# Kernel tuning notes

Measured on AMD Instinct MI355X. Metric: run time of the kernel, lower is better.

## Reference

```python
import jax, jax.numpy as jnp
import numpy as np

B, TE, TD, D, U = 8, 256, 256, 256, 256


def setup_inputs() -> dict:
    key = jax.random.key(0)
    k1, k2, k3, k4, k5 = jax.random.split(key, 5)
    glorot = lambda k, shape: jax.random.uniform(
        k, shape, jnp.float32,
        -np.sqrt(6.0 / (shape[0] + shape[1])), np.sqrt(6.0 / (shape[0] + shape[1])))
    return {
        "en_seq": jax.random.normal(k1, (B, TE, D), jnp.float32),
        "de_seq": jax.random.normal(k2, (B, TD, D), jnp.float32),
        "w_en": glorot(k3, (D, U)),
        "w_de": glorot(k4, (D, U)),
        "nu": glorot(k5, (U, 1)),
    }


def reference(en_seq, de_seq, w_en, w_de, nu):
    # Additive co-attention scores.
    ae = jnp.einsum('bte,eu->btu', en_seq, w_en)          # (B, Te, U)
    ad = jnp.einsum('bsd,du->bsu', de_seq, w_de)          # (B, Td, U)
    # co_m[b, td, te, u] = ae[b, te, u] + ad[b, td, u]  (matches K.repeat / repeat_elements layout)
    co = jnp.tanh(ad[:, :, None, :] + ae[:, None, :, :])  # (B, Td, Te, U)
    mu = jnp.einsum('bstu,ul->bst', co, nu)               # (B, Td, Te)
    alphas = jax.nn.softmax(mu, axis=-1)                  # softmax over en time
    max_mu = jnp.max(mu, axis=-1)                         # (B, Td)
    max_alphas = jax.nn.softmax(max_mu, axis=-1)          # softmax over de time
    h_hat = jnp.sum(de_seq * max_alphas[..., None], axis=1)  # (B, Dd)
    sum_en = jnp.einsum('bst,bte->bse', alphas, en_seq)      # (B, Td, De)
    output = jnp.concatenate(
        [de_seq, sum_en, de_seq * sum_en, de_seq * h_hat[:, None, :]], axis=-1)
    return output  # (B, Td, 4*D)
```

## Files before the change

### kernel.cpp

```cpp
#include <hip/hip_runtime.h>

#define B_   8
#define TE_  256
#define TD_  256
#define D_   256
#define U_   256

#define EET_OFF   0
#define ED_OFF    524288
#define ALPHA_OFF 1048576
#define MAXMU_OFF 1572864
#define HH_OFF    1574912

__device__ __forceinline__ float fexp2(float x) {
#if __has_builtin(__builtin_amdgcn_exp2f)
  return __builtin_amdgcn_exp2f(x);
#else
  return exp2f(x);
#endif
}
__device__ __forceinline__ float frcp(float x) {
#if __has_builtin(__builtin_amdgcn_rcpf)
  return __builtin_amdgcn_rcpf(x);
#else
  return 1.0f / x;
#endif
}
__device__ __forceinline__ float rdlane(float v, int l) {
  return __int_as_float(__builtin_amdgcn_readlane(__float_as_int(v), l));
}

#define LOG2E_F 1.4426950408889634f
#define TWO_LOG2E_F 2.8853900817779268f

__global__ __launch_bounds__(256) void coatt_k1_proj(
    const float* __restrict__ en, const float* __restrict__ de,
    const float* __restrict__ w_en, const float* __restrict__ w_de,
    float* __restrict__ ws) {
  const int bi = blockIdx.x;
  const int which = bi >> 8;
  const float* __restrict__ A = which ? de : en;
  const float* __restrict__ W = which ? w_de : w_en;
  const int r0 = (bi & 255) * 8;
  const int tid = threadIdx.x;
  const int w = tid >> 6, lane = tid & 63;
  const int rowW = r0 + w * 2;
  const int u4 = lane * 4;

  const float* __restrict__ Arow = A + (size_t)(rowW + (lane >> 5)) * D_ + (lane & 31);

  float4 acc0 = {0, 0, 0, 0}, acc1 = {0, 0, 0, 0};
  for (int k0 = 0; k0 < D_; k0 += 32) {
    const float areg = Arow[k0];
#pragma unroll
    for (int h = 0; h < 2; ++h) {
      float4 wv[16];
#pragma unroll
      for (int k = 0; k < 16; ++k)
        wv[k] = *(const float4*)&W[(k0 + h * 16 + k) * U_ + u4];
#pragma unroll
      for (int k = 0; k < 16; ++k) {
        const float a0 = rdlane(areg, h * 16 + k);
        const float a1 = rdlane(areg, 32 + h * 16 + k);
        acc0.x = fmaf(a0, wv[k].x, acc0.x);
        acc0.y = fmaf(a0, wv[k].y, acc0.y);
        acc0.z = fmaf(a0, wv[k].z, acc0.z);
        acc0.w = fmaf(a0, wv[k].w, acc0.w);
        acc1.x = fmaf(a1, wv[k].x, acc1.x);
        acc1.y = fmaf(a1, wv[k].y, acc1.y);
        acc1.z = fmaf(a1, wv[k].z, acc1.z);
        acc1.w = fmaf(a1, wv[k].w, acc1.w);
      }
    }
  }

  __shared__ float TT[8][257];
  if (which) {
    float* __restrict__ out = ws + ED_OFF;
    float4 o0, o1;
    o0.x = fexp2(acc0.x * TWO_LOG2E_F); o0.y = fexp2(acc0.y * TWO_LOG2E_F);
    o0.z = fexp2(acc0.z * TWO_LOG2E_F); o0.w = fexp2(acc0.w * TWO_LOG2E_F);
    o1.x = fexp2(acc1.x * TWO_LOG2E_F); o1.y = fexp2(acc1.y * TWO_LOG2E_F);
    o1.z = fexp2(acc1.z * TWO_LOG2E_F); o1.w = fexp2(acc1.w * TWO_LOG2E_F);
    *(float4*)&out[(rowW + 0) * U_ + u4] = o0;
    *(float4*)&out[(rowW + 1) * U_ + u4] = o1;
  } else {
    const float* a0p = (const float*)&acc0;
    const float* a1p = (const float*)&acc1;
#pragma unroll
    for (int j = 0; j < 4; ++j) {
      TT[w * 2 + 0][u4 + j] = fexp2(a0p[j] * TWO_LOG2E_F);
      TT[w * 2 + 1][u4 + j] = fexp2(a1p[j] * TWO_LOG2E_F);
    }
    __syncthreads();
    const int b = r0 >> 8, t0 = r0 & 255;
    float v[8];
#pragma unroll
    for (int k = 0; k < 8; ++k) v[k] = TT[k][tid];
    float* __restrict__ p = ws + EET_OFF + (size_t)(b * U_ + tid) * TE_ + t0;
    float4 q0, q1;
    q0.x = v[0]; q0.y = v[1]; q0.z = v[2]; q0.w = v[3];
    q1.x = v[4]; q1.y = v[5]; q1.z = v[6]; q1.w = v[7];
    *(float4*)&p[0] = q0;
    *(float4*)&p[4] = q1;
  }
}

__global__ __launch_bounds__(256) void coatt_k2_mu(
    const float* __restrict__ nu, float* __restrict__ ws) {
  float* __restrict__ alphas = ws + ALPHA_OFF;
  float* __restrict__ maxmu = ws + MAXMU_OFF;
  const int b = blockIdx.y;
  const int sBase = blockIdx.x * 4;
  const int tid = threadIdx.x;
  const int w = tid >> 6, lane = tid & 63;
  const float* __restrict__ Ee_b = ws + EET_OFF + (size_t)b * U_ * TE_ + tid;
  const float* __restrict__ EdCoop =
      ws + ED_OFF + (size_t)(b * TD_ + sBase + (lane >> 4)) * U_ + (lane & 15);

  float acc0 = 0.f, acc1 = 0.f, acc2 = 0.f, acc3 = 0.f;
  for (int c = 0; c < 4; ++c) {
    const float nureg = nu[c * 64 + lane];
#pragma unroll
    for (int q = 0; q < 4; ++q) {
      const int u0 = c * 64 + q * 16;
      const float edreg = EdCoop[u0];
      float ee[16];
#pragma unroll
      for (int j = 0; j < 16; ++j) ee[j] = Ee_b[(u0 + j) * TE_];
#pragma unroll
      for (int j = 0; j < 16; ++j) {
        const float nv = rdlane(nureg, q * 16 + j);
        const float e0 = rdlane(edreg, j);
        const float e1 = rdlane(edreg, 16 + j);
        const float e2 = rdlane(edreg, 32 + j);
        const float e3 = rdlane(edreg, 48 + j);
        acc0 = fmaf(nv, frcp(fmaf(e0, ee[j], 1.0f)), acc0);
        acc1 = fmaf(nv, frcp(fmaf(e1, ee[j], 1.0f)), acc1);
        acc2 = fmaf(nv, frcp(fmaf(e2, ee[j], 1.0f)), acc2);
        acc3 = fmaf(nv, frcp(fmaf(e3, ee[j], 1.0f)), acc3);
      }
    }
  }
  float v[4] = {-2.f * acc0, -2.f * acc1, -2.f * acc2, -2.f * acc3};
  __shared__ float part[4][4];
  float m[4];
#pragma unroll
  for (int s = 0; s < 4; ++s) {
    m[s] = v[s];
#pragma unroll
    for (int off = 32; off > 0; off >>= 1) m[s] = fmaxf(m[s], __shfl_xor(m[s], off));
    if (lane == 0) part[s][w] = m[s];
  }
  __syncthreads();
#pragma unroll
  for (int s = 0; s < 4; ++s)
    m[s] = fmaxf(fmaxf(part[s][0], part[s][1]), fmaxf(part[s][2], part[s][3]));
  __syncthreads();
  float e[4], sm[4];
#pragma unroll
  for (int s = 0; s < 4; ++s) {
    e[s] = fexp2((v[s] - m[s]) * LOG2E_F);
    sm[s] = e[s];
#pragma unroll
    for (int off = 32; off > 0; off >>= 1) sm[s] += __shfl_xor(sm[s], off);
    if (lane == 0) part[s][w] = sm[s];
  }
  __syncthreads();
  float* __restrict__ al = alphas + (size_t)(b * TD_ + sBase) * TE_;
#pragma unroll
  for (int s = 0; s < 4; ++s) {
    const float tot = (part[s][0] + part[s][1]) + (part[s][2] + part[s][3]);
    al[s * TE_ + tid] = e[s] * frcp(tot);
  }
  if (tid == 0) {
#pragma unroll
    for (int s = 0; s < 4; ++s) maxmu[b * TD_ + sBase + s] = m[s];
  }
}

__global__ __launch_bounds__(256) void coatt_k3_hhat(
    const float* __restrict__ de, float* __restrict__ ws) {
  const float* __restrict__ maxmu = ws + MAXMU_OFF;
  float* __restrict__ hhat = ws + HH_OFF;
  const int b = blockIdx.y;
  const int dBase = blockIdx.x * 32;
  const int tid = threadIdx.x;
  const int w = tid >> 6, lane = tid & 63;
  __shared__ float red[8];
  __shared__ float malpha[256];
  __shared__ float acc_red[256];
  const float v = maxmu[b * TD_ + tid];
  float m = v;
#pragma unroll
  for (int off = 32; off > 0; off >>= 1) m = fmaxf(m, __shfl_xor(m, off));
  if (lane == 0) red[w] = m;
  __syncthreads();
  m = fmaxf(fmaxf(red[0], red[1]), fmaxf(red[2], red[3]));
  const float e = fexp2((v - m) * LOG2E_F);
  float sm = e;
#pragma unroll
  for (int off = 32; off > 0; off >>= 1) sm += __shfl_xor(sm, off);
  if (lane == 0) red[4 + w] = sm;
  __syncthreads();
  sm = (red[4] + red[5]) + (red[6] + red[7]);
  malpha[tid] = e * frcp(sm);
  __syncthreads();
  const int dl = tid & 31, sg = tid >> 5;
  float acc = 0.f;
  for (int s = sg * 32; s < sg * 32 + 32; ++s)
    acc = fmaf(de[(b * TD_ + s) * D_ + dBase + dl], malpha[s], acc);
  acc_red[tid] = acc;
  __syncthreads();
  if (tid < 32) {
    float t = acc_red[tid];
#pragma unroll
    for (int g = 1; g < 8; ++g) t += acc_red[g * 32 + tid];
    hhat[b * D_ + dBase + tid] = t;
  }
}

__global__ __launch_bounds__(256) void coatt_k4_out(
    const float* __restrict__ en, const float* __restrict__ de,
    const float* __restrict__ ws, float* __restrict__ out) {
  const float* __restrict__ hhat = ws + HH_OFF;
  const int b = blockIdx.y;
  const int sBase = blockIdx.x * 4;
  const int tid = threadIdx.x;
  const int lane = tid & 63;
  const int d = tid;
  const float* __restrict__ alCoop =
      ws + ALPHA_OFF + (size_t)(b * TD_ + sBase + (lane >> 4)) * TE_ + (lane & 15);
  const float* __restrict__ en_b = en + (size_t)b * TE_ * D_ + d;

  float acc0 = 0.f, acc1 = 0.f, acc2 = 0.f, acc3 = 0.f;
  for (int t0 = 0; t0 < TE_; t0 += 16) {
    const float alreg = alCoop[t0];
    float env[16];
#pragma unroll
    for (int j = 0; j < 16; ++j) env[j] = en_b[(t0 + j) * D_];
#pragma unroll
    for (int j = 0; j < 16; ++j) {
      acc0 = fmaf(rdlane(alreg, j),      env[j], acc0);
      acc1 = fmaf(rdlane(alreg, 16 + j), env[j], acc1);
      acc2 = fmaf(rdlane(alreg, 32 + j), env[j], acc2);
      acc3 = fmaf(rdlane(alreg, 48 + j), env[j], acc3);
    }
  }
  const float hh = hhat[b * D_ + d];
  const float se[4] = {acc0, acc1, acc2, acc3};
#pragma unroll
  for (int s = 0; s < 4; ++s) {
    const float dd = de[(size_t)(b * TD_ + sBase + s) * D_ + d];
    float* o = out + (size_t)(b * TD_ + sBase + s) * (4 * D_);
    o[d] = dd;
    o[D_ + d] = se[s];
    o[2 * D_ + d] = dd * se[s];
    o[3 * D_ + d] = dd * hh;
  }
}

extern "C" void kernel_launch(void* const* d_in, const int* in_sizes, int n_in,
                              void* d_out, int out_size, void* d_ws, size_t ws_size,
                              hipStream_t stream) {
  (void)in_sizes; (void)n_in; (void)out_size; (void)ws_size;
  const float* en   = (const float*)d_in[0];
  const float* de   = (const float*)d_in[1];
  const float* w_en = (const float*)d_in[2];
  const float* w_de = (const float*)d_in[3];
  const float* nu   = (const float*)d_in[4];
  float* out = (float*)d_out;
  float* ws  = (float*)d_ws;

  coatt_k1_proj<<<dim3(512), 256, 0, stream>>>(en, de, w_en, w_de, ws);
  coatt_k2_mu<<<dim3(64, 8), 256, 0, stream>>>(nu, ws);
  coatt_k3_hhat<<<dim3(8, 8), 256, 0, stream>>>(de, ws);
  coatt_k4_out<<<dim3(64, 8), 256, 0, stream>>>(en, de, ws, out);
}
```

Before: 138.7 us.

## Fuse h_hat into output kernel and software-pipeline loads in all kernels

Removes the separate h_hat kernel. Each output block now recomputes the max-mu softmax and the weighted de-sum redundantly, which saves a launch and a dependency step but adds 256x256 extra reads per block. The projection, mu and output kernels gain register double-buffering so the next tile's loads are issued before the current tile's FMAs. Cross-lane readlane broadcasts are replaced with uniform float4 loads of Ed, nu and alpha, and launch bounds now ask for 2 blocks per SIMD.

```diff
diff --git a/kernel.cpp b/kernel.cpp
--- a/kernel.cpp
+++ b/kernel.cpp
@@ -10,7 +10,6 @@
 #define ED_OFF    524288
 #define ALPHA_OFF 1048576
 #define MAXMU_OFF 1572864
-#define HH_OFF    1574912
 
 __device__ __forceinline__ float fexp2(float x) {
 #if __has_builtin(__builtin_amdgcn_exp2f)
@@ -33,7 +32,7 @@
 #define LOG2E_F 1.4426950408889634f
 #define TWO_LOG2E_F 2.8853900817779268f
 
-__global__ __launch_bounds__(256) void coatt_k1_proj(
+__global__ __launch_bounds__(256, 2) void coatt_k1_proj(
     const float* __restrict__ en, const float* __restrict__ de,
     const float* __restrict__ w_en, const float* __restrict__ w_de,
     float* __restrict__ ws) {
@@ -50,28 +49,37 @@
   const float* __restrict__ Arow = A + (size_t)(rowW + (lane >> 5)) * D_ + (lane & 31);
 
   float4 acc0 = {0, 0, 0, 0}, acc1 = {0, 0, 0, 0};
-  for (int k0 = 0; k0 < D_; k0 += 32) {
-    const float areg = Arow[k0];
-#pragma unroll
-    for (int h = 0; h < 2; ++h) {
-      float4 wv[16];
-#pragma unroll
-      for (int k = 0; k < 16; ++k)
-        wv[k] = *(const float4*)&W[(k0 + h * 16 + k) * U_ + u4];
-#pragma unroll
-      for (int k = 0; k < 16; ++k) {
-        const float a0 = rdlane(areg, h * 16 + k);
-        const float a1 = rdlane(areg, 32 + h * 16 + k);
-        acc0.x = fmaf(a0, wv[k].x, acc0.x);
-        acc0.y = fmaf(a0, wv[k].y, acc0.y);
-        acc0.z = fmaf(a0, wv[k].z, acc0.z);
-        acc0.w = fmaf(a0, wv[k].w, acc0.w);
-        acc1.x = fmaf(a1, wv[k].x, acc1.x);
-        acc1.y = fmaf(a1, wv[k].y, acc1.y);
-        acc1.z = fmaf(a1, wv[k].z, acc1.z);
-        acc1.w = fmaf(a1, wv[k].w, acc1.w);
+  float areg = Arow[0];
+  float4 wbuf[8], wnxt[8];
+#pragma unroll
+  for (int j = 0; j < 8; ++j) wbuf[j] = *(const float4*)&W[j * U_ + u4];
+
+  for (int win = 0; win < 8; ++win) {
+    const float aNxt = Arow[((win + 1) & 7) * 32];
+#pragma unroll
+    for (int q = 0; q < 4; ++q) {
+      const int kb = win * 32 + q * 8;
+      const int kn = (kb + 8) & 255;
+#pragma unroll
+      for (int j = 0; j < 8; ++j)
+        wnxt[j] = *(const float4*)&W[(kn + j) * U_ + u4];
+#pragma unroll
+      for (int k = 0; k < 8; ++k) {
+        const float a0 = rdlane(areg, q * 8 + k);
+        const float a1 = rdlane(areg, 32 + q * 8 + k);
+        acc0.x = fmaf(a0, wbuf[k].x, acc0.x);
+        acc0.y = fmaf(a0, wbuf[k].y, acc0.y);
+        acc0.z = fmaf(a0, wbuf[k].z, acc0.z);
+        acc0.w = fmaf(a0, wbuf[k].w, acc0.w);
+        acc1.x = fmaf(a1, wbuf[k].x, acc1.x);
+        acc1.y = fmaf(a1, wbuf[k].y, acc1.y);
+        acc1.z = fmaf(a1, wbuf[k].z, acc1.z);
+        acc1.w = fmaf(a1, wbuf[k].w, acc1.w);
       }
-    }
+#pragma unroll
+      for (int j = 0; j < 8; ++j) wbuf[j] = wnxt[j];
+    }
+    areg = aNxt;
   }
 
   __shared__ float TT[8][257];
@@ -106,7 +114,7 @@
   }
 }
 
-__global__ __launch_bounds__(256) void coatt_k2_mu(
+__global__ __launch_bounds__(256, 2) void coatt_k2_mu(
     const float* __restrict__ nu, float* __restrict__ ws) {
   float* __restrict__ alphas = ws + ALPHA_OFF;
   float* __restrict__ maxmu = ws + MAXMU_OFF;
@@ -115,32 +123,40 @@
   const int tid = threadIdx.x;
   const int w = tid >> 6, lane = tid & 63;
   const float* __restrict__ Ee_b = ws + EET_OFF + (size_t)b * U_ * TE_ + tid;
-  const float* __restrict__ EdCoop =
-      ws + ED_OFF + (size_t)(b * TD_ + sBase + (lane >> 4)) * U_ + (lane & 15);
+  const float* __restrict__ Ed_b = ws + ED_OFF + (size_t)(b * TD_ + sBase) * U_;
+
+  float ee[16], een[16];
+#pragma unroll
+  for (int j = 0; j < 16; ++j) ee[j] = Ee_b[j * TE_];
 
   float acc0 = 0.f, acc1 = 0.f, acc2 = 0.f, acc3 = 0.f;
-  for (int c = 0; c < 4; ++c) {
-    const float nureg = nu[c * 64 + lane];
+  for (int u0 = 0; u0 < U_; u0 += 16) {
+    const int un = (u0 + 16) & 255;
+#pragma unroll
+    for (int j = 0; j < 16; ++j) een[j] = Ee_b[(un + j) * TE_];
 #pragma unroll
     for (int q = 0; q < 4; ++q) {
-      const int u0 = c * 64 + q * 16;
-      const float edreg = EdCoop[u0];
-      float ee[16];
-#pragma unroll
-      for (int j = 0; j < 16; ++j) ee[j] = Ee_b[(u0 + j) * TE_];
-#pragma unroll
-      for (int j = 0; j < 16; ++j) {
-        const float nv = rdlane(nureg, q * 16 + j);
-        const float e0 = rdlane(edreg, j);
-        const float e1 = rdlane(edreg, 16 + j);
-        const float e2 = rdlane(edreg, 32 + j);
-        const float e3 = rdlane(edreg, 48 + j);
-        acc0 = fmaf(nv, frcp(fmaf(e0, ee[j], 1.0f)), acc0);
-        acc1 = fmaf(nv, frcp(fmaf(e1, ee[j], 1.0f)), acc1);
-        acc2 = fmaf(nv, frcp(fmaf(e2, ee[j], 1.0f)), acc2);
-        acc3 = fmaf(nv, frcp(fmaf(e3, ee[j], 1.0f)), acc3);
+      const float4 nv = *(const float4*)&nu[u0 + q * 4];
+      const float4 e0 = *(const float4*)&Ed_b[0 * U_ + u0 + q * 4];
+      const float4 e1 = *(const float4*)&Ed_b[1 * U_ + u0 + q * 4];
+      const float4 e2 = *(const float4*)&Ed_b[2 * U_ + u0 + q * 4];
+      const float4 e3 = *(const float4*)&Ed_b[3 * U_ + u0 + q * 4];
+      const float* nvp = (const float*)&nv;
+      const float* p0 = (const float*)&e0;
+      const float* p1 = (const float*)&e1;
+      const float* p2 = (const float*)&e2;
+      const float* p3 = (const float*)&e3;
+#pragma unroll
+      for (int j = 0; j < 4; ++j) {
+        const float eev = ee[q * 4 + j];
+        acc0 = fmaf(nvp[j], frcp(fmaf(p0[j], eev, 1.0f)), acc0);
+        acc1 = fmaf(nvp[j], frcp(fmaf(p1[j], eev, 1.0f)), acc1);
+        acc2 = fmaf(nvp[j], frcp(fmaf(p2[j], eev, 1.0f)), acc2);
+        acc3 = fmaf(nvp[j], frcp(fmaf(p3[j], eev, 1.0f)), acc3);
       }
     }
+#pragma unroll
+    for (int j = 0; j < 16; ++j) ee[j] = een[j];
   }
   float v[4] = {-2.f * acc0, -2.f * acc1, -2.f * acc2, -2.f * acc3};
   __shared__ float part[4][4];
@@ -179,75 +195,73 @@
   }
 }
 
-__global__ __launch_bounds__(256) void coatt_k3_hhat(
-    const float* __restrict__ de, float* __restrict__ ws) {
-  const float* __restrict__ maxmu = ws + MAXMU_OFF;
-  float* __restrict__ hhat = ws + HH_OFF;
-  const int b = blockIdx.y;
-  const int dBase = blockIdx.x * 32;
-  const int tid = threadIdx.x;
-  const int w = tid >> 6, lane = tid & 63;
-  __shared__ float red[8];
-  __shared__ float malpha[256];
-  __shared__ float acc_red[256];
-  const float v = maxmu[b * TD_ + tid];
-  float m = v;
-#pragma unroll
-  for (int off = 32; off > 0; off >>= 1) m = fmaxf(m, __shfl_xor(m, off));
-  if (lane == 0) red[w] = m;
-  __syncthreads();
-  m = fmaxf(fmaxf(red[0], red[1]), fmaxf(red[2], red[3]));
-  const float e = fexp2((v - m) * LOG2E_F);
-  float sm = e;
-#pragma unroll
-  for (int off = 32; off > 0; off >>= 1) sm += __shfl_xor(sm, off);
-  if (lane == 0) red[4 + w] = sm;
-  __syncthreads();
-  sm = (red[4] + red[5]) + (red[6] + red[7]);
-  malpha[tid] = e * frcp(sm);
-  __syncthreads();
-  const int dl = tid & 31, sg = tid >> 5;
-  float acc = 0.f;
-  for (int s = sg * 32; s < sg * 32 + 32; ++s)
-    acc = fmaf(de[(b * TD_ + s) * D_ + dBase + dl], malpha[s], acc);
-  acc_red[tid] = acc;
-  __syncthreads();
-  if (tid < 32) {
-    float t = acc_red[tid];
-#pragma unroll
-    for (int g = 1; g < 8; ++g) t += acc_red[g * 32 + tid];
-    hhat[b * D_ + dBase + tid] = t;
-  }
-}
-
-__global__ __launch_bounds__(256) void coatt_k4_out(
+__global__ __launch_bounds__(256, 2) void coatt_k4_out(
     const float* __restrict__ en, const float* __restrict__ de,
     const float* __restrict__ ws, float* __restrict__ out) {
-  const float* __restrict__ hhat = ws + HH_OFF;
+  const float* __restrict__ maxmu = ws + MAXMU_OFF;
   const int b = blockIdx.y;
   const int sBase = blockIdx.x * 4;
   const int tid = threadIdx.x;
   const int lane = tid & 63;
   const int d = tid;
-  const float* __restrict__ alCoop =
-      ws + ALPHA_OFF + (size_t)(b * TD_ + sBase + (lane >> 4)) * TE_ + (lane & 15);
+
+  float4 mv = *(const float4*)&maxmu[b * TD_ + lane * 4];
+  float mx = fmaxf(fmaxf(mv.x, mv.y), fmaxf(mv.z, mv.w));
+#pragma unroll
+  for (int off = 32; off > 0; off >>= 1) mx = fmaxf(mx, __shfl_xor(mx, off));
+  float4 ex;
+  ex.x = fexp2((mv.x - mx) * LOG2E_F);
+  ex.y = fexp2((mv.y - mx) * LOG2E_F);
+  ex.z = fexp2((mv.z - mx) * LOG2E_F);
+  ex.w = fexp2((mv.w - mx) * LOG2E_F);
+  float ss = (ex.x + ex.y) + (ex.z + ex.w);
+#pragma unroll
+  for (int off = 32; off > 0; off >>= 1) ss += __shfl_xor(ss, off);
+  const float inv = frcp(ss);
+  float mal[4] = {ex.x * inv, ex.y * inv, ex.z * inv, ex.w * inv};
+
+  const float* __restrict__ de_b = de + (size_t)b * TD_ * D_ + d;
+  float hh = 0.f;
+#pragma unroll 8
+  for (int s4 = 0; s4 < 64; ++s4) {
+#pragma unroll
+    for (int c = 0; c < 4; ++c)
+      hh = fmaf(de_b[(s4 * 4 + c) * D_], rdlane(mal[c], s4), hh);
+  }
+
+  const float* __restrict__ al = ws + ALPHA_OFF + (size_t)(b * TD_ + sBase) * TE_;
   const float* __restrict__ en_b = en + (size_t)b * TE_ * D_ + d;
-
+  float env[16], envn[16];
+#pragma unroll
+  for (int j = 0; j < 16; ++j) env[j] = en_b[j * D_];
   float acc0 = 0.f, acc1 = 0.f, acc2 = 0.f, acc3 = 0.f;
   for (int t0 = 0; t0 < TE_; t0 += 16) {
-    const float alreg = alCoop[t0];
-    float env[16];
-#pragma unroll
-    for (int j = 0; j < 16; ++j) env[j] = en_b[(t0 + j) * D_];
-#pragma unroll
-    for (int j = 0; j < 16; ++j) {
-      acc0 = fmaf(rdlane(alreg, j),      env[j], acc0);
-      acc1 = fmaf(rdlane(alreg, 16 + j), env[j], acc1);
-      acc2 = fmaf(rdlane(alreg, 32 + j), env[j], acc2);
-      acc3 = fmaf(rdlane(alreg, 48 + j), env[j], acc3);
-    }
-  }
-  const float hh = hhat[b * D_ + d];
+    const int tn = (t0 + 16) & 255;
+#pragma unroll
+    for (int j = 0; j < 16; ++j) envn[j] = en_b[(tn + j) * D_];
+#pragma unroll
+    for (int q = 0; q < 4; ++q) {
+      const float4 a0 = *(const float4*)&al[0 * TE_ + t0 + q * 4];
+      const float4 a1 = *(const float4*)&al[1 * TE_ + t0 + q * 4];
+      const float4 a2 = *(const float4*)&al[2 * TE_ + t0 + q * 4];
+      const float4 a3 = *(const float4*)&al[3 * TE_ + t0 + q * 4];
+      const float* q0 = (const float*)&a0;
+      const float* q1 = (const float*)&a1;
+      const float* q2 = (const float*)&a2;
+      const float* q3 = (const float*)&a3;
+#pragma unroll
+      for (int j = 0; j < 4; ++j) {
+        const float e = env[q * 4 + j];
+        acc0 = fmaf(q0[j], e, acc0);
+        acc1 = fmaf(q1[j], e, acc1);
+        acc2 = fmaf(q2[j], e, acc2);
+        acc3 = fmaf(q3[j], e, acc3);
+      }
+    }
+#pragma unroll
+    for (int j = 0; j < 16; ++j) env[j] = envn[j];
+  }
+
   const float se[4] = {acc0, acc1, acc2, acc3};
 #pragma unroll
   for (int s = 0; s < 4; ++s) {
@@ -274,6 +288,5 @@
 
   coatt_k1_proj<<<dim3(512), 256, 0, stream>>>(en, de, w_en, w_de, ws);
   coatt_k2_mu<<<dim3(64, 8), 256, 0, stream>>>(nu, ws);
-  coatt_k3_hhat<<<dim3(8, 8), 256, 0, stream>>>(de, ws);
   coatt_k4_out<<<dim3(64, 8), 256, 0, stream>>>(en, de, ws, out);
 }
```

Result: faster. 128.9 us (-7.1%).
